# Kernel tuning notes

Hardware: AMD Instinct MI355X
Metric: run time of the kernel (lower is better)

Reference implementation:

```python
import jax, jax.numpy as jnp
import numpy as np

B, N, D = 16, 4096, 256
S = 8            # num_slots
ITERS = 3
H = 256          # mlp hidden = max(dim, 256)
SCALE = D ** -0.5
TEMP = 1.0
LN_EPS = 1e-5


def _ln(x, g, b):
    mu = jnp.mean(x, axis=-1, keepdims=True)
    var = jnp.var(x, axis=-1, keepdims=True)
    return (x - mu) * jax.lax.rsqrt(var + LN_EPS) * g + b


def setup_inputs() -> dict:
    key = jax.random.key(0)
    ks = jax.random.split(key, 16)
    xav = float(np.sqrt(6.0 / (S * D + D)))  # xavier_uniform over (1,S,D)
    lin = float(np.sqrt(1.0 / D))
    return {
        "embeddings": jax.random.normal(ks[0], (B, N, D), jnp.float32),
        "slots_noise": jax.random.normal(ks[1], (1, S, D), jnp.float32) * 0.0 + jax.random.normal(ks[1], (B, S, D), jnp.float32),
        "slots_mu": jax.random.uniform(ks[2], (1, S, D), jnp.float32, -xav, xav),
        "slots_logsigma": jax.random.uniform(ks[3], (1, S, D), jnp.float32, -xav, xav),
        "Wk": jax.random.uniform(ks[4], (S, D, D), jnp.float32, -lin, lin),
        "Wq": jax.random.uniform(ks[5], (D, D), jnp.float32, -lin, lin),
        "Wv": jax.random.uniform(ks[6], (S, D, D), jnp.float32, -lin, lin),
        "W_ih": jax.random.uniform(ks[7], (3 * D, D), jnp.float32, -lin, lin),
        "W_hh": jax.random.uniform(ks[8], (3 * D, D), jnp.float32, -lin, lin),
        "b_ih": jax.random.uniform(ks[9], (3 * D,), jnp.float32, -lin, lin),
        "b_hh": jax.random.uniform(ks[10], (3 * D,), jnp.float32, -lin, lin),
        "W1": jax.random.uniform(ks[11], (H, D), jnp.float32, -lin, lin),
        "b1": jnp.zeros((H,), jnp.float32),
        "W2": jax.random.uniform(ks[12], (D, H), jnp.float32, -float(np.sqrt(1.0 / H)), float(np.sqrt(1.0 / H))),
        "b2": jnp.zeros((D,), jnp.float32),
        "g_in": jnp.ones((D,), jnp.float32), "be_in": jnp.zeros((D,), jnp.float32),
        "g_s": jnp.ones((D,), jnp.float32), "be_s": jnp.zeros((D,), jnp.float32),
        "g_ff": jnp.ones((D,), jnp.float32), "be_ff": jnp.zeros((D,), jnp.float32),
    }


def _gru(x, h, W_ih, W_hh, b_ih, b_hh):
    # torch.nn.GRUCell math; x,h: [M, D]
    gi = x @ W_ih.T + b_ih
    gh = h @ W_hh.T + b_hh
    i_r, i_z, i_n = jnp.split(gi, 3, axis=-1)
    h_r, h_z, h_n = jnp.split(gh, 3, axis=-1)
    r = jax.nn.sigmoid(i_r + h_r)
    z = jax.nn.sigmoid(i_z + h_z)
    n = jnp.tanh(i_n + r * h_n)
    return (1.0 - z) * n + z * h


def reference(embeddings, slots_noise, slots_mu, slots_logsigma, Wk, Wq, Wv,
              W_ih, W_hh, b_ih, b_hh, W1, b1, W2, b2,
              g_in, be_in, g_s, be_s, g_ff, be_ff):
    b, n, d = embeddings.shape
    slots = slots_mu + jnp.exp(slots_logsigma) * slots_noise   # [B,S,D]
    emb = _ln(embeddings, g_in, be_in)                          # [B,N,D]
    # per-slot keys / values: keys[s] = emb @ Wk[s].T  -> [S,B,N,D]
    keys = jnp.einsum('bnd,sed->sbne', emb, Wk)
    values = jnp.einsum('bnd,sed->sbne', emb, Wv)

    attn_vis = None
    for _ in range(ITERS):
        slots_prev = slots
        slots_n = _ln(slots, g_s, be_s)
        q = jnp.einsum('bsd,ed->bse', slots_n, Wq)              # [B,S,D]
        dots = jnp.einsum('bsd,sbnd->bsn', q, keys) * SCALE     # [B,S,N]
        attn = jax.nn.softmax(dots / TEMP, axis=1)              # softmax over slots
        attn_vis = attn
        attn_w = attn / jnp.sum(attn, axis=-1, keepdims=True)   # normalize over tokens
        updates = jnp.einsum('sbnd,bsn->bsd', values, attn_w)   # [B,S,D]
        h = _gru(updates.reshape(b * S, d), slots_prev.reshape(b * S, d),
                 W_ih, W_hh, b_ih, b_hh).reshape(b, S, d)
        ff = _ln(h, g_ff, be_ff)
        slots = h + (jax.nn.relu(ff @ W1.T + b1) @ W2.T + b2)
    return slots, attn_vis
```

## Files before the change

### kernel.cpp

```cpp
#include <hip/hip_runtime.h>

#define DEVI __device__ __forceinline__

constexpr float SCALE = 0.0625f;
constexpr float LN_EPS = 1e-5f;

DEVI float dot8f(const float* __restrict__ w, const float* __restrict__ x){
  float4 a = *(const float4*)w;
  float4 b = *(const float4*)(w + 4);
  return a.x*x[0]+a.y*x[1]+a.z*x[2]+a.w*x[3]+b.x*x[4]+b.y*x[5]+b.z*x[6]+b.w*x[7];
}

DEVI float gemv256(const float* __restrict__ W, const float* __restrict__ xv,
                   float (*part)[33], int tid){
  const int c8 = tid & 31, ep = tid >> 5;
  float xs8[8];
  #pragma unroll
  for (int j = 0; j < 8; ++j) xs8[j] = xv[c8*8 + j];
  const float* Wb = W + c8*8;
  #pragma unroll 4
  for (int ei = 0; ei < 32; ++ei){
    int e = ep*32 + ei;
    part[e][c8] = dot8f(Wb + (size_t)e*256, xs8);
  }
  __syncthreads();
  float acc = 0.f;
  #pragma unroll
  for (int p = 0; p < 32; ++p) acc += part[tid][p];
  return acc;
}

DEVI float block_ln(float x, const float* __restrict__ g, const float* __restrict__ be,
                    float* red, int tid, int lane, int wv){
  float v1 = x, v2 = x*x;
  #pragma unroll
  for (int o = 32; o; o >>= 1){ v1 += __shfl_xor(v1,o,64); v2 += __shfl_xor(v2,o,64); }
  if (lane == 0){ red[wv] = v1; red[4+wv] = v2; }
  __syncthreads();
  float mu = (red[0]+red[1]+red[2]+red[3]) * (1.f/256.f);
  float var = (red[4]+red[5]+red[6]+red[7]) * (1.f/256.f) - mu*mu;
  float inv = rsqrtf(var + LN_EPS);
  float r = (x - mu)*inv*g[tid] + be[tid];
  __syncthreads();
  return r;
}

__global__ void k_init(const float* __restrict__ noise, const float* __restrict__ smu,
                       const float* __restrict__ slsig, float* __restrict__ slotsA,
                       float* __restrict__ uacc, float* __restrict__ Zacc){
  const int r = blockIdx.x, tid = threadIdx.x, s = r & 7;
  slotsA[r*256 + tid] = smu[s*256 + tid] + expf(slsig[s*256 + tid]) * noise[r*256 + tid];
  uacc[r*256 + tid] = 0.f;
  if (tid == 0) Zacc[r] = 0.f;
}

__global__ __launch_bounds__(256) void kS1(const float* __restrict__ slots_in,
    const float* __restrict__ uacc, const float* __restrict__ Zacc,
    const float* __restrict__ Wv, const float* __restrict__ W_hh,
    float* __restrict__ upd, float* __restrict__ gh){
  __shared__ float xv[256];
  __shared__ float part[256][33];
  const int m = blockIdx.x;
  const int r = blockIdx.y, tid = threadIdx.x, s = r & 7;
  const float* W   = (m == 0) ? (Wv + (size_t)s*65536) : (W_hh + (size_t)(m-1)*65536);
  const float* src = (m == 0) ? (uacc + r*256) : (slots_in + r*256);
  xv[tid] = src[tid];
  __syncthreads();
  float acc = gemv256(W, xv, part, tid);
  if (m == 0) upd[r*256 + tid] = acc * (1.f / Zacc[r]);
  else        gh[((m-1)*128 + r)*256 + tid] = acc;
}

__global__ __launch_bounds__(256) void kS2(const float* __restrict__ upd,
    const float* __restrict__ W_ih, const float* __restrict__ b_ih,
    float* __restrict__ gi, float* __restrict__ uacc, float* __restrict__ Zacc){
  __shared__ float xv[256];
  __shared__ float part[256][33];
  const int g = blockIdx.x, r = blockIdx.y, tid = threadIdx.x;
  xv[tid] = upd[r*256 + tid];
  if (g == 0) uacc[r*256 + tid] = 0.f;
  if (g == 1 && tid == 0) Zacc[r] = 0.f;
  __syncthreads();
  float acc = gemv256(W_ih + (size_t)g*65536, xv, part, tid);
  gi[(g*128 + r)*256 + tid] = acc + b_ih[g*256 + tid];
}

__global__ __launch_bounds__(256) void kS3(const float* __restrict__ slots_in,
    const float* __restrict__ gi, const float* __restrict__ gh,
    const float* __restrict__ b_hh,
    const float* __restrict__ g_ff, const float* __restrict__ be_ff,
    const float* __restrict__ W1, const float* __restrict__ b1,
    float* __restrict__ hbuf, float* __restrict__ hid){
  __shared__ float xv[256];
  __shared__ float part[256][33];
  __shared__ float red[8];
  const int r = blockIdx.x, tid = threadIdx.x;
  const int lane = tid & 63, wv = tid >> 6;
  float i_r = gi[(0*128 + r)*256 + tid];
  float i_z = gi[(1*128 + r)*256 + tid];
  float i_n = gi[(2*128 + r)*256 + tid];
  float h_r = gh[(0*128 + r)*256 + tid] + b_hh[tid];
  float h_z = gh[(1*128 + r)*256 + tid] + b_hh[256 + tid];
  float h_n = gh[(2*128 + r)*256 + tid] + b_hh[512 + tid];
  float hp = slots_in[r*256 + tid];
  float rg = 1.f/(1.f + expf(-(i_r + h_r)));
  float zg = 1.f/(1.f + expf(-(i_z + h_z)));
  float ng = tanhf(i_n + rg*h_n);
  float h = (1.f - zg)*ng + zg*hp;
  hbuf[r*256 + tid] = h;
  float lnh = block_ln(h, g_ff, be_ff, red, tid, lane, wv);
  xv[tid] = lnh;
  __syncthreads();
  float acc = gemv256(W1, xv, part, tid);
  hid[r*256 + tid] = fmaxf(acc + b1[tid], 0.f);
}

__global__ __launch_bounds__(256) void kS4(const float* __restrict__ hid,
    const float* __restrict__ hbuf, const float* __restrict__ W2,
    const float* __restrict__ b2, float* __restrict__ slots_out,
    float* __restrict__ out_slots, int last){
  __shared__ float xv[256];
  __shared__ float part[256][33];
  const int r = blockIdx.x, tid = threadIdx.x;
  xv[tid] = hid[r*256 + tid];
  __syncthreads();
  float acc = gemv256(W2, xv, part, tid);
  float out = hbuf[r*256 + tid] + acc + b2[tid];
  slots_out[r*256 + tid] = out;
  if (last) out_slots[r*256 + tid] = out;
}

__global__ __launch_bounds__(256) void kS5(const float* __restrict__ slots,
    const float* __restrict__ g_s, const float* __restrict__ be_s,
    const float* __restrict__ Wq, float* __restrict__ qbuf){
  __shared__ float xv[256];
  __shared__ float part[256][33];
  __shared__ float red[8];
  const int r = blockIdx.x, tid = threadIdx.x;
  const int lane = tid & 63, wv = tid >> 6;
  float x = slots[r*256 + tid];
  float sn = block_ln(x, g_s, be_s, red, tid, lane, wv);
  xv[tid] = sn;
  __syncthreads();
  qbuf[r*256 + tid] = gemv256(Wq, xv, part, tid);
}

__global__ __launch_bounds__(256) void kS6(const float* __restrict__ qbuf,
    const float* __restrict__ Wk,
    const float* __restrict__ g_in, const float* __restrict__ be_in,
    float* __restrict__ qg, float* __restrict__ gqbq){
  __shared__ float xv[256];
  __shared__ float partK[8][256];
  __shared__ float red[8];
  const int r = blockIdx.x, tid = threadIdx.x, s = r & 7;
  const int lane = tid & 63, wv = tid >> 6;
  xv[tid] = qbuf[r*256 + tid];
  __syncthreads();
  const int c8 = tid & 31, ep = tid >> 5;
  float acc8[8];
  #pragma unroll
  for (int j = 0; j < 8; ++j) acc8[j] = 0.f;
  const float* Wb = Wk + ((size_t)s*256)*256 + c8*8;
  #pragma unroll 4
  for (int ei = 0; ei < 32; ++ei){
    int e = ep*32 + ei;
    const float* wp = Wb + (size_t)e*256;
    float4 wa = *(const float4*)wp;
    float4 wb = *(const float4*)(wp + 4);
    float qe = xv[e];
    acc8[0] += qe*wa.x; acc8[1] += qe*wa.y; acc8[2] += qe*wa.z; acc8[3] += qe*wa.w;
    acc8[4] += qe*wb.x; acc8[5] += qe*wb.y; acc8[6] += qe*wb.z; acc8[7] += qe*wb.w;
  }
  float* pk = &partK[ep][c8*8];
  #pragma unroll
  for (int j = 0; j < 8; ++j) pk[j] = acc8[j];
  __syncthreads();
  float qk = 0.f;
  #pragma unroll
  for (int p = 0; p < 8; ++p) qk += partK[p][tid];
  float qgv = qk * g_in[tid] * SCALE;
  float bqv = qk * be_in[tid] * SCALE;
  qg[r*256 + tid] = qgv;
  float vq = qgv, vb = bqv;
  #pragma unroll
  for (int o = 32; o; o >>= 1){ vq += __shfl_xor(vq,o,64); vb += __shfl_xor(vb,o,64); }
  if (lane == 0){ red[wv] = vq; red[4+wv] = vb; }
  __syncthreads();
  if (tid == 0) gqbq[r*2+0] = red[0]+red[1]+red[2]+red[3];
  if (tid == 1) gqbq[r*2+1] = red[4]+red[5]+red[6]+red[7];
}

__global__ __launch_bounds__(256) void k_main(const float* __restrict__ emb,
    const float* __restrict__ qg, const float* __restrict__ gqbq,
    const float* __restrict__ g_in, const float* __restrict__ be_in,
    float* __restrict__ uacc, float* __restrict__ Zacc,
    float* __restrict__ out_attn, int write_attn){
  __shared__ float U[8192];
  float* const qgL = U;
  float* const avL = U + 2048;
  float4* const Sp4 = (float4*)U;
  __shared__ float aL[512];
  __shared__ float red2[2][8][4];
  __shared__ float Zs[8], A2s[8], GqL[8], BqL[8];

  const int tid = threadIdx.x, lane = tid & 63, wv = tid >> 6;
  const int blk = blockIdx.x, b = blk >> 6, tile = blk & 63;
  const int n0 = tile * 64;

  {
    const float4* src = (const float4*)(qg + (size_t)b * 2048);
    float4* dst = (float4*)qgL;
    #pragma unroll
    for (int k = 0; k < 2; ++k){
      int w = tid + k*256;
      int s = w >> 6, f = w & 63, qq = f >> 3, j = f & 7;
      dst[s*64 + qq*8 + ((j + qq) & 7)] = src[w];
    }
  }
  if (tid < 8){
    GqL[tid] = gqbq[(b*8 + tid)*2 + 0];
    BqL[tid] = gqbq[(b*8 + tid)*2 + 1];
  }
  __syncthreads();

  const int qq = tid & 7;
  float zsum[8], z2sum[8];
  #pragma unroll
  for (int s = 0; s < 8; ++s){ zsum[s] = 0.f; z2sum[s] = 0.f; }

  #pragma unroll
  for (int pass = 0; pass < 2; ++pass){
    const int t = pass*32 + (tid >> 3);
    const float4* xrow = (const float4*)(emb + ((size_t)(b*4096 + n0 + t))*256 + qq*32);
    float4 xv4[8];
    #pragma unroll
    for (int j = 0; j < 8; ++j) xv4[j] = xrow[j];
    float s1 = 0.f, s2 = 0.f, acc[8];
    #pragma unroll
    for (int s = 0; s < 8; ++s) acc[s] = 0.f;
    #pragma unroll
    for (int j = 0; j < 8; ++j){
      float4 u = xv4[j];
      s1 += (u.x+u.y)+(u.z+u.w);
      s2 += u.x*u.x+u.y*u.y+u.z*u.z+u.w*u.w;
      const float* qb = qgL + qq*32 + ((j + qq) & 7)*4;
      #pragma unroll
      for (int s = 0; s < 8; ++s){
        float4 q0 = *(const float4*)(qb + s*256);
        acc[s] += u.x*q0.x + u.y*q0.y + u.z*q0.z + u.w*q0.w;
      }
    }
    #pragma unroll
    for (int o = 1; o <= 4; o <<= 1){
      s1 += __shfl_xor(s1,o,64); s2 += __shfl_xor(s2,o,64);
      #pragma unroll
      for (int s = 0; s < 8; ++s) acc[s] += __shfl_xor(acc[s],o,64);
    }
    float mu = s1 * (1.f/256.f);
    float var = s2 * (1.f/256.f) - mu*mu;
    float inv = rsqrtf(var + LN_EPS);
    float dv[8], mx = -1e30f;
    #pragma unroll
    for (int s = 0; s < 8; ++s){
      dv[s] = inv * (acc[s] - mu * GqL[s]) + BqL[s];
      mx = fmaxf(mx, dv[s]);
    }
    float den = 0.f;
    #pragma unroll
    for (int s = 0; s < 8; ++s){ dv[s] = expf(dv[s] - mx); den += dv[s]; }
    float rden = 1.f / den;
    #pragma unroll
    for (int s = 0; s < 8; ++s){
      float at = dv[s] * rden;
      float av = at * inv;
      if (qq == 0){ avL[s*64 + t] = at; aL[s*64 + t] = av; }
      zsum[s] += at;
      z2sum[s] += av * mu;
    }
  }
  #pragma unroll
  for (int s = 0; s < 8; ++s){
    #pragma unroll
    for (int o = 32; o; o >>= 1){
      zsum[s] += __shfl_xor(zsum[s], o, 64);
      z2sum[s] += __shfl_xor(z2sum[s], o, 64);
    }
  }
  if (lane == 0){
    #pragma unroll
    for (int s = 0; s < 8; ++s){ red2[0][s][wv] = zsum[s]*0.125f; red2[1][s][wv] = z2sum[s]*0.125f; }
  }
  __syncthreads();
  if (tid < 8){
    Zs[tid]  = red2[0][tid][0]+red2[0][tid][1]+red2[0][tid][2]+red2[0][tid][3];
    A2s[tid] = red2[1][tid][0]+red2[1][tid][1]+red2[1][tid][2]+red2[1][tid][3];
  }
  if (write_attn){
    int s = tid >> 5, tk = tid & 31;
    #pragma unroll
    for (int p = 0; p < 2; ++p)
      out_attn[((size_t)(b*8 + s))*4096 + n0 + p*32 + tk] = avL[s*64 + p*32 + tk];
  }
  __syncthreads();
  {
    const int r4 = tid >> 6, cq = tid & 63;
    float4 S1[8];
    #pragma unroll
    for (int s = 0; s < 8; ++s) S1[s] = make_float4(0.f,0.f,0.f,0.f);
    const float4* xbase = (const float4*)(emb + ((size_t)(b*4096 + n0))*256) + cq;
    #pragma unroll 4
    for (int i = 0; i < 16; ++i){
      int t = r4 + i*4;
      float4 x4 = xbase[t*64];
      #pragma unroll
      for (int s = 0; s < 8; ++s){
        float a = aL[s*64 + t];
        S1[s].x += a*x4.x; S1[s].y += a*x4.y; S1[s].z += a*x4.z; S1[s].w += a*x4.w;
      }
    }
    #pragma unroll
    for (int s = 0; s < 8; ++s) Sp4[(r4*8 + s)*64 + cq] = S1[s];
  }
  __syncthreads();
  {
    const int c = tid;
    const float* Sp = (const float*)Sp4;
    float gc = g_in[c], bc = be_in[c];
    float* dst = uacc + ((size_t)b*8)*256 + c;
    #pragma unroll
    for (int si = 0; si < 8; ++si){
      int s = (si + blk) & 7;
      float v = Sp[(0*8+s)*256 + c] + Sp[(1*8+s)*256 + c]
              + Sp[(2*8+s)*256 + c] + Sp[(3*8+s)*256 + c];
      atomicAdd(&dst[s*256], gc * (v - A2s[s]) + bc * Zs[s]);
    }
    if (tid < 8) atomicAdd(&Zacc[b*8 + tid], Zs[tid]);
  }
}

extern "C" void kernel_launch(void* const* d_in, const int* in_sizes, int n_in,
                              void* d_out, int out_size, void* d_ws, size_t ws_size,
                              hipStream_t stream){
  const float* emb   = (const float*)d_in[0];
  const float* noise = (const float*)d_in[1];
  const float* smu   = (const float*)d_in[2];
  const float* slsig = (const float*)d_in[3];
  const float* Wk    = (const float*)d_in[4];
  const float* Wq    = (const float*)d_in[5];
  const float* Wv    = (const float*)d_in[6];
  const float* W_ih  = (const float*)d_in[7];
  const float* W_hh  = (const float*)d_in[8];
  const float* b_ih  = (const float*)d_in[9];
  const float* b_hh  = (const float*)d_in[10];
  const float* W1    = (const float*)d_in[11];
  const float* b1    = (const float*)d_in[12];
  const float* W2    = (const float*)d_in[13];
  const float* b2    = (const float*)d_in[14];
  const float* g_in  = (const float*)d_in[15];
  const float* be_in = (const float*)d_in[16];
  const float* g_s   = (const float*)d_in[17];
  const float* be_s  = (const float*)d_in[18];
  const float* g_ff  = (const float*)d_in[19];
  const float* be_ff = (const float*)d_in[20];

  float* ws     = (float*)d_ws;
  float* slotsA = ws;
  float* slotsB = ws + 32768;
  float* qg     = ws + 65536;
  float* gqbq   = ws + 98304;
  float* uacc   = ws + 98560;
  float* Zacc   = ws + 131328;
  float* upd    = ws + 131456;
  float* gh     = ws + 164224;
  float* gi     = ws + 262528;
  float* hbuf   = ws + 360832;
  float* hid    = ws + 393600;
  float* qbuf   = ws + 426368;

  float* out_slots = (float*)d_out;
  float* out_attn  = out_slots + 32768;
  const int has_attn = (out_size >= 32768 + 16*8*4096);

  k_init<<<dim3(128), dim3(256), 0, stream>>>(noise, smu, slsig, slotsA, uacc, Zacc);
  kS5<<<dim3(128), dim3(256), 0, stream>>>(slotsA, g_s, be_s, Wq, qbuf);
  kS6<<<dim3(128), dim3(256), 0, stream>>>(qbuf, Wk, g_in, be_in, qg, gqbq);
  for (int it = 0; it < 3; ++it){
    int last = (it == 2);
    float* sin  = (it == 1) ? slotsB : slotsA;
    float* sout = (it == 1) ? slotsA : slotsB;
    k_main<<<dim3(1024), dim3(256), 0, stream>>>(emb, qg, gqbq, g_in, be_in,
        uacc, Zacc, out_attn, last && has_attn);
    kS1<<<dim3(4,128), dim3(256), 0, stream>>>(sin, uacc, Zacc, Wv, W_hh, upd, gh);
    kS2<<<dim3(3,128), dim3(256), 0, stream>>>(upd, W_ih, b_ih, gi, uacc, Zacc);
    kS3<<<dim3(128), dim3(256), 0, stream>>>(sin, gi, gh, b_hh, g_ff, be_ff, W1, b1, hbuf, hid);
    kS4<<<dim3(128), dim3(256), 0, stream>>>(hid, hbuf, W2, b2, sout, out_slots, last);
    if (!last){
      kS5<<<dim3(128), dim3(256), 0, stream>>>(sout, g_s, be_s, Wq, qbuf);
      kS6<<<dim3(128), dim3(256), 0, stream>>>(qbuf, Wk, g_in, be_in, qg, gqbq);
    }
  }
}
```

Baseline: 326.6 us.

## Fuse slot-update GEMV chain into two kernels per iteration

Merges the six small per-iteration kernels (Wv/W_hh GEMV, W_ih GEMV, GRU+W1, W2, LN+Wq, Wk projection) into two kernels, k_updA and k_updB, plus a fused init+query kernel. This removes launch overhead and the global round-trips for intermediates such as upd, gi, gh, hid and qbuf. In exchange, each block now runs up to seven GEMVs serially over only 128 blocks, down from up to 512 in parallel, so there is less parallelism on the weight-streaming work.

```diff
diff --git a/kernel.cpp b/kernel.cpp
--- a/kernel.cpp
+++ b/kernel.cpp
@@ -45,117 +45,21 @@
   return r;
 }
 
-__global__ void k_init(const float* __restrict__ noise, const float* __restrict__ smu,
-                       const float* __restrict__ slsig, float* __restrict__ slotsA,
-                       float* __restrict__ uacc, float* __restrict__ Zacc){
-  const int r = blockIdx.x, tid = threadIdx.x, s = r & 7;
-  slotsA[r*256 + tid] = smu[s*256 + tid] + expf(slsig[s*256 + tid]) * noise[r*256 + tid];
-  uacc[r*256 + tid] = 0.f;
-  if (tid == 0) Zacc[r] = 0.f;
-}
-
-__global__ __launch_bounds__(256) void kS1(const float* __restrict__ slots_in,
-    const float* __restrict__ uacc, const float* __restrict__ Zacc,
-    const float* __restrict__ Wv, const float* __restrict__ W_hh,
-    float* __restrict__ upd, float* __restrict__ gh){
-  __shared__ float xv[256];
-  __shared__ float part[256][33];
-  const int m = blockIdx.x;
-  const int r = blockIdx.y, tid = threadIdx.x, s = r & 7;
-  const float* W   = (m == 0) ? (Wv + (size_t)s*65536) : (W_hh + (size_t)(m-1)*65536);
-  const float* src = (m == 0) ? (uacc + r*256) : (slots_in + r*256);
-  xv[tid] = src[tid];
-  __syncthreads();
-  float acc = gemv256(W, xv, part, tid);
-  if (m == 0) upd[r*256 + tid] = acc * (1.f / Zacc[r]);
-  else        gh[((m-1)*128 + r)*256 + tid] = acc;
-}
-
-__global__ __launch_bounds__(256) void kS2(const float* __restrict__ upd,
-    const float* __restrict__ W_ih, const float* __restrict__ b_ih,
-    float* __restrict__ gi, float* __restrict__ uacc, float* __restrict__ Zacc){
-  __shared__ float xv[256];
-  __shared__ float part[256][33];
-  const int g = blockIdx.x, r = blockIdx.y, tid = threadIdx.x;
-  xv[tid] = upd[r*256 + tid];
-  if (g == 0) uacc[r*256 + tid] = 0.f;
-  if (g == 1 && tid == 0) Zacc[r] = 0.f;
-  __syncthreads();
-  float acc = gemv256(W_ih + (size_t)g*65536, xv, part, tid);
-  gi[(g*128 + r)*256 + tid] = acc + b_ih[g*256 + tid];
-}
-
-__global__ __launch_bounds__(256) void kS3(const float* __restrict__ slots_in,
-    const float* __restrict__ gi, const float* __restrict__ gh,
-    const float* __restrict__ b_hh,
-    const float* __restrict__ g_ff, const float* __restrict__ be_ff,
-    const float* __restrict__ W1, const float* __restrict__ b1,
-    float* __restrict__ hbuf, float* __restrict__ hid){
-  __shared__ float xv[256];
-  __shared__ float part[256][33];
-  __shared__ float red[8];
-  const int r = blockIdx.x, tid = threadIdx.x;
+DEVI void qproj(float sval, int r, int s, int tid,
+                const float* __restrict__ g_s, const float* __restrict__ be_s,
+                const float* __restrict__ Wq, const float* __restrict__ Wk,
+                const float* __restrict__ g_in, const float* __restrict__ be_in,
+                float* __restrict__ qg, float* __restrict__ gqbq,
+                float* xv, float (*part)[33], float* red){
   const int lane = tid & 63, wv = tid >> 6;
-  float i_r = gi[(0*128 + r)*256 + tid];
-  float i_z = gi[(1*128 + r)*256 + tid];
-  float i_n = gi[(2*128 + r)*256 + tid];
-  float h_r = gh[(0*128 + r)*256 + tid] + b_hh[tid];
-  float h_z = gh[(1*128 + r)*256 + tid] + b_hh[256 + tid];
-  float h_n = gh[(2*128 + r)*256 + tid] + b_hh[512 + tid];
-  float hp = slots_in[r*256 + tid];
-  float rg = 1.f/(1.f + expf(-(i_r + h_r)));
-  float zg = 1.f/(1.f + expf(-(i_z + h_z)));
-  float ng = tanhf(i_n + rg*h_n);
-  float h = (1.f - zg)*ng + zg*hp;
-  hbuf[r*256 + tid] = h;
-  float lnh = block_ln(h, g_ff, be_ff, red, tid, lane, wv);
-  xv[tid] = lnh;
-  __syncthreads();
-  float acc = gemv256(W1, xv, part, tid);
-  hid[r*256 + tid] = fmaxf(acc + b1[tid], 0.f);
-}
-
-__global__ __launch_bounds__(256) void kS4(const float* __restrict__ hid,
-    const float* __restrict__ hbuf, const float* __restrict__ W2,
-    const float* __restrict__ b2, float* __restrict__ slots_out,
-    float* __restrict__ out_slots, int last){
-  __shared__ float xv[256];
-  __shared__ float part[256][33];
-  const int r = blockIdx.x, tid = threadIdx.x;
-  xv[tid] = hid[r*256 + tid];
-  __syncthreads();
-  float acc = gemv256(W2, xv, part, tid);
-  float out = hbuf[r*256 + tid] + acc + b2[tid];
-  slots_out[r*256 + tid] = out;
-  if (last) out_slots[r*256 + tid] = out;
-}
-
-__global__ __launch_bounds__(256) void kS5(const float* __restrict__ slots,
-    const float* __restrict__ g_s, const float* __restrict__ be_s,
-    const float* __restrict__ Wq, float* __restrict__ qbuf){
-  __shared__ float xv[256];
-  __shared__ float part[256][33];
-  __shared__ float red[8];
-  const int r = blockIdx.x, tid = threadIdx.x;
-  const int lane = tid & 63, wv = tid >> 6;
-  float x = slots[r*256 + tid];
-  float sn = block_ln(x, g_s, be_s, red, tid, lane, wv);
+  float sn = block_ln(sval, g_s, be_s, red, tid, lane, wv);
   xv[tid] = sn;
   __syncthreads();
-  qbuf[r*256 + tid] = gemv256(Wq, xv, part, tid);
-}
-
-__global__ __launch_bounds__(256) void kS6(const float* __restrict__ qbuf,
-    const float* __restrict__ Wk,
-    const float* __restrict__ g_in, const float* __restrict__ be_in,
-    float* __restrict__ qg, float* __restrict__ gqbq){
-  __shared__ float xv[256];
-  __shared__ float partK[8][256];
-  __shared__ float red[8];
-  const int r = blockIdx.x, tid = threadIdx.x, s = r & 7;
-  const int lane = tid & 63, wv = tid >> 6;
-  xv[tid] = qbuf[r*256 + tid];
-  __syncthreads();
+  float q = gemv256(Wq, xv, part, tid);
+  __syncthreads();
+  xv[tid] = q;
+  __syncthreads();
+  float* partK = &part[0][0];
   const int c8 = tid & 31, ep = tid >> 5;
   float acc8[8];
   #pragma unroll
@@ -171,13 +75,13 @@
     acc8[0] += qe*wa.x; acc8[1] += qe*wa.y; acc8[2] += qe*wa.z; acc8[3] += qe*wa.w;
     acc8[4] += qe*wb.x; acc8[5] += qe*wb.y; acc8[6] += qe*wb.z; acc8[7] += qe*wb.w;
   }
-  float* pk = &partK[ep][c8*8];
+  float* pk = partK + ep*256 + c8*8;
   #pragma unroll
   for (int j = 0; j < 8; ++j) pk[j] = acc8[j];
   __syncthreads();
   float qk = 0.f;
   #pragma unroll
-  for (int p = 0; p < 8; ++p) qk += partK[p][tid];
+  for (int p = 0; p < 8; ++p) qk += partK[p*256 + tid];
   float qgv = qk * g_in[tid] * SCALE;
   float bqv = qk * be_in[tid] * SCALE;
   qg[r*256 + tid] = qgv;
@@ -188,6 +92,95 @@
   __syncthreads();
   if (tid == 0) gqbq[r*2+0] = red[0]+red[1]+red[2]+red[3];
   if (tid == 1) gqbq[r*2+1] = red[4]+red[5]+red[6]+red[7];
+}
+
+__global__ __launch_bounds__(256) void k_initq(const float* __restrict__ noise,
+    const float* __restrict__ smu, const float* __restrict__ slsig,
+    float* __restrict__ slotsA, float* __restrict__ uacc, float* __restrict__ Zacc,
+    const float* __restrict__ g_s, const float* __restrict__ be_s,
+    const float* __restrict__ Wq, const float* __restrict__ Wk,
+    const float* __restrict__ g_in, const float* __restrict__ be_in,
+    float* __restrict__ qg, float* __restrict__ gqbq){
+  __shared__ float xv[256];
+  __shared__ float part[256][33];
+  __shared__ float red[8];
+  const int r = blockIdx.x, tid = threadIdx.x, s = r & 7;
+  float sl = smu[s*256 + tid] + expf(slsig[s*256 + tid]) * noise[r*256 + tid];
+  slotsA[r*256 + tid] = sl;
+  uacc[r*256 + tid] = 0.f;
+  if (tid == 0) Zacc[r] = 0.f;
+  qproj(sl, r, s, tid, g_s, be_s, Wq, Wk, g_in, be_in, qg, gqbq, xv, part, red);
+}
+
+__global__ __launch_bounds__(256) void k_updA(const float* __restrict__ sin_,
+    float* __restrict__ uacc, float* __restrict__ Zacc,
+    const float* __restrict__ Wv, const float* __restrict__ W_ih,
+    const float* __restrict__ W_hh,
+    const float* __restrict__ b_ih, const float* __restrict__ b_hh,
+    float* __restrict__ hbuf){
+  __shared__ float xv[256];
+  __shared__ float part[256][33];
+  const int r = blockIdx.x, tid = threadIdx.x, s = r & 7;
+
+  float rZ = 1.f / Zacc[r];
+  xv[tid] = uacc[r*256 + tid];
+  uacc[r*256 + tid] = 0.f;
+  __syncthreads();
+  float upd = gemv256(Wv + (size_t)s*65536, xv, part, tid) * rZ;
+  if (tid == 0) Zacc[r] = 0.f;
+
+  float hp = sin_[r*256 + tid];
+  xv[tid] = hp;
+  __syncthreads();
+  float hr_ = gemv256(W_hh,          xv, part, tid) + b_hh[tid];
+  __syncthreads();
+  float hz_ = gemv256(W_hh +  65536, xv, part, tid) + b_hh[256 + tid];
+  __syncthreads();
+  float hn_ = gemv256(W_hh + 131072, xv, part, tid) + b_hh[512 + tid];
+
+  xv[tid] = upd;
+  __syncthreads();
+  float ir_ = gemv256(W_ih,          xv, part, tid) + b_ih[tid];
+  __syncthreads();
+  float iz_ = gemv256(W_ih +  65536, xv, part, tid) + b_ih[256 + tid];
+  __syncthreads();
+  float in_ = gemv256(W_ih + 131072, xv, part, tid) + b_ih[512 + tid];
+
+  float rg = 1.f/(1.f + expf(-(ir_ + hr_)));
+  float zg = 1.f/(1.f + expf(-(iz_ + hz_)));
+  float ng = tanhf(in_ + rg*hn_);
+  hbuf[r*256 + tid] = (1.f - zg)*ng + zg*hp;
+}
+
+__global__ __launch_bounds__(256) void k_updB(const float* __restrict__ hbuf,
+    float* __restrict__ sout,
+    const float* __restrict__ g_ff, const float* __restrict__ be_ff,
+    const float* __restrict__ W1, const float* __restrict__ b1,
+    const float* __restrict__ W2, const float* __restrict__ b2,
+    const float* __restrict__ g_s, const float* __restrict__ be_s,
+    const float* __restrict__ Wq, const float* __restrict__ Wk,
+    const float* __restrict__ g_in, const float* __restrict__ be_in,
+    float* __restrict__ qg, float* __restrict__ gqbq,
+    float* __restrict__ out_slots, int last){
+  __shared__ float xv[256];
+  __shared__ float part[256][33];
+  __shared__ float red[8];
+  const int r = blockIdx.x, tid = threadIdx.x, s = r & 7;
+  const int lane = tid & 63, wv = tid >> 6;
+
+  float h = hbuf[r*256 + tid];
+  float lnh = block_ln(h, g_ff, be_ff, red, tid, lane, wv);
+  xv[tid] = lnh;
+  __syncthreads();
+  float hid = fmaxf(gemv256(W1, xv, part, tid) + b1[tid], 0.f);
+  __syncthreads();
+  xv[tid] = hid;
+  __syncthreads();
+  float out = h + gemv256(W2, xv, part, tid) + b2[tid];
+  sout[r*256 + tid] = out;
+  if (last){ out_slots[r*256 + tid] = out; return; }
+
+  qproj(out, r, s, tid, g_s, be_s, Wq, Wk, g_in, be_in, qg, gqbq, xv, part, red);
 }
 
 __global__ __launch_bounds__(256) void k_main(const float* __restrict__ emb,
@@ -370,33 +363,24 @@
   float* gqbq   = ws + 98304;
   float* uacc   = ws + 98560;
   float* Zacc   = ws + 131328;
-  float* upd    = ws + 131456;
-  float* gh     = ws + 164224;
-  float* gi     = ws + 262528;
-  float* hbuf   = ws + 360832;
-  float* hid    = ws + 393600;
-  float* qbuf   = ws + 426368;
+  float* hbuf   = ws + 131456;
 
   float* out_slots = (float*)d_out;
   float* out_attn  = out_slots + 32768;
   const int has_attn = (out_size >= 32768 + 16*8*4096);
 
-  k_init<<<dim3(128), dim3(256), 0, stream>>>(noise, smu, slsig, slotsA, uacc, Zacc);
-  kS5<<<dim3(128), dim3(256), 0, stream>>>(slotsA, g_s, be_s, Wq, qbuf);
-  kS6<<<dim3(128), dim3(256), 0, stream>>>(qbuf, Wk, g_in, be_in, qg, gqbq);
+  k_initq<<<dim3(128), dim3(256), 0, stream>>>(noise, smu, slsig, slotsA, uacc, Zacc,
+      g_s, be_s, Wq, Wk, g_in, be_in, qg, gqbq);
   for (int it = 0; it < 3; ++it){
     int last = (it == 2);
     float* sin  = (it == 1) ? slotsB : slotsA;
     float* sout = (it == 1) ? slotsA : slotsB;
     k_main<<<dim3(1024), dim3(256), 0, stream>>>(emb, qg, gqbq, g_in, be_in,
         uacc, Zacc, out_attn, last && has_attn);
-    kS1<<<dim3(4,128), dim3(256), 0, stream>>>(sin, uacc, Zacc, Wv, W_hh, upd, gh);
-    kS2<<<dim3(3,128), dim3(256), 0, stream>>>(upd, W_ih, b_ih, gi, uacc, Zacc);
-    kS3<<<dim3(128), dim3(256), 0, stream>>>(sin, gi, gh, b_hh, g_ff, be_ff, W1, b1, hbuf, hid);
-    kS4<<<dim3(128), dim3(256), 0, stream>>>(hid, hbuf, W2, b2, sout, out_slots, last);
-    if (!last){
-      kS5<<<dim3(128), dim3(256), 0, stream>>>(sout, g_s, be_s, Wq, qbuf);
-      kS6<<<dim3(128), dim3(256), 0, stream>>>(qbuf, Wk, g_in, be_in, qg, gqbq);
-    }
-  }
-}
+    k_updA<<<dim3(128), dim3(256), 0, stream>>>(sin, uacc, Zacc,
+        Wv, W_ih, W_hh, b_ih, b_hh, hbuf);
+    k_updB<<<dim3(128), dim3(256), 0, stream>>>(hbuf, sout,
+        g_ff, be_ff, W1, b1, W2, b2,
+        g_s, be_s, Wq, Wk, g_in, be_in, qg, gqbq, out_slots, last);
+  }
+}
```

Measured after the change: 408.1 us. 24.9% more time.
